# Optimization experiments

Hardware: AMD Instinct MI355X
Metric: run time of the kernel (lower is better)

Reference implementation:

```python
import jax, jax.numpy as jnp
import numpy as np

N, E, D, H = 100000, 600000, 128, 512  # nodes, edges, latent_dim, 4*latent_dim


def setup_inputs() -> dict:
    key = jax.random.key(0)
    ks = jax.random.split(key, 9)
    s = 0.05
    return {
        "z": jax.random.normal(ks[0], (N, D), dtype=jnp.float32),
        "edge_index": jax.random.randint(ks[1], (2, E), 0, N, dtype=jnp.int64),
        "Wg": jax.random.normal(ks[2], (D, D), dtype=jnp.float32) * s,
        "Ws": jax.random.normal(ks[3], (D, D), dtype=jnp.float32) * s,
        "bg": jnp.zeros((D,), dtype=jnp.float32),
        "W1": jax.random.normal(ks[4], (D, H), dtype=jnp.float32) * s,
        "b1": jnp.zeros((H,), dtype=jnp.float32),
        "W2": jax.random.normal(ks[5], (H, H), dtype=jnp.float32) * s,
        "b2": jnp.zeros((H,), dtype=jnp.float32),
        "W3": jax.random.normal(ks[6], (H, D), dtype=jnp.float32) * s,
        "b3": jnp.zeros((D,), dtype=jnp.float32),
    }


def reference(z, edge_index, Wg, Ws, bg, W1, b1, W2, b2, W3, b3):
    src, dst = edge_index[0], edge_index[1]
    n = z.shape[0]
    # GNN: gather neighbor features along edges, mean-aggregate at dst
    msgs = z[src]                                   # (E, D) gather
    agg = jax.ops.segment_sum(msgs, dst, num_segments=n)  # (N, D) scatter-add
    deg = jax.ops.segment_sum(jnp.ones((src.shape[0],), z.dtype), dst, num_segments=n)
    agg = agg / jnp.maximum(deg, 1.0)[:, None]      # mean aggregation
    h = jax.nn.relu(agg @ Wg + z @ Ws + bg)          # (N, D) graph conv output
    # MLP: Linear -> Tanh -> Linear -> Tanh -> Linear
    h = jnp.tanh(h @ W1 + b1)
    h = jnp.tanh(h @ W2 + b2)
    return h @ W3 + b3                               # dz/dt: (N, D)
```

## Files before the change

### kernel.cpp

```cpp
#include <hip/hip_runtime.h>
#include <hip/hip_fp16.h>


typedef _Float16 f16;
typedef __attribute__((ext_vector_type(4))) _Float16 f16x4;
typedef __attribute__((ext_vector_type(8))) _Float16 f16x8;
typedef __attribute__((ext_vector_type(4))) float f32x4;

__device__ __forceinline__ void async_load16(const void* g, void* lds) {
  __builtin_amdgcn_global_load_lds(
      (const __attribute__((address_space(1))) void*)g,
      (__attribute__((address_space(3))) void*)lds, 16, 0, 0);
}

__device__ __forceinline__ float fast_tanh(float x) {
  float a = fabsf(x);
  float e = __expf(-2.0f * a);
  float r = (1.0f - e) * __builtin_amdgcn_rcpf(1.0f + e);
  return copysignf(r, x);
}

__global__ __launch_bounds__(256) void zero_kernel(int* __restrict__ p, int n) {
  int i = blockIdx.x * 256 + threadIdx.x;
  int stride = gridDim.x * 256;
  for (; i < n; i += stride) p[i] = 0;
}

__global__ __launch_bounds__(256) void scan_partial(const int* __restrict__ degi,
                                                    int* __restrict__ bsum, int N) {
  __shared__ int lds[256];
  int b = blockIdx.x, t = threadIdx.x;
  int s = 0;
#pragma unroll
  for (int j = 0; j < 4; ++j) {
    int idx = b * 1024 + t * 4 + j;
    if (idx < N) s += degi[idx];
  }
  lds[t] = s;
  __syncthreads();
  for (int off = 128; off > 0; off >>= 1) {
    if (t < off) lds[t] += lds[t + off];
    __syncthreads();
  }
  if (t == 0) bsum[b] = lds[0];
}

__global__ void scan_bsums(const int* __restrict__ bsum, int* __restrict__ boff,
                           int* __restrict__ row_start, int nb, int N) {
  if (threadIdx.x == 0 && blockIdx.x == 0) {
    int acc = 0;
    for (int i = 0; i < nb; ++i) { boff[i] = acc; acc += bsum[i]; }
    row_start[N] = acc;
  }
}

__global__ __launch_bounds__(256) void scan_final(
    const int* __restrict__ degi, const int* __restrict__ boff,
    int* __restrict__ row_start, int* __restrict__ cursor, int N) {
  __shared__ int lds[256];
  int b = blockIdx.x, t = threadIdx.x;
  int base = b * 1024;
  int v[4];
  int s = 0;
#pragma unroll
  for (int j = 0; j < 4; ++j) {
    int idx = base + t * 4 + j;
    v[j] = (idx < N) ? degi[idx] : 0;
    s += v[j];
  }
  lds[t] = s;
  __syncthreads();
  for (int off = 1; off < 256; off <<= 1) {
    int x = lds[t];
    int y = (t >= off) ? lds[t - off] : 0;
    __syncthreads();
    lds[t] = x + y;
    __syncthreads();
  }
  int pre = boff[b] + lds[t] - s;
#pragma unroll
  for (int j = 0; j < 4; ++j) {
    int idx = base + t * 4 + j;
    if (idx < N) { row_start[idx] = pre; cursor[idx] = pre; pre += v[j]; }
  }
}

__global__ __launch_bounds__(256) void fill_adj(const int* __restrict__ src,
                                                const int* __restrict__ dst,
                                                int* __restrict__ cursor,
                                                int* __restrict__ adj, int E) {
  int e = blockIdx.x * 256 + threadIdx.x;
  if (e >= E) return;
  int p = atomicAdd(&cursor[dst[e]], 1);
  adj[p] = src[e];
}

__global__ __launch_bounds__(256) void fused_prep(
    const int* __restrict__ dst, int* __restrict__ degi, int E,
    const float* __restrict__ Wg, const float* __restrict__ Ws,
    const float* __restrict__ W1, const float* __restrict__ W2,
    const float* __restrict__ W3, f16* __restrict__ wgs, f16* __restrict__ wt1,
    f16* __restrict__ wt2, f16* __restrict__ wt3,
    const float* __restrict__ z, f16* __restrict__ z16, f16* __restrict__ Xc,
    int n4) {
  int i0 = blockIdx.x * 256 + threadIdx.x;
  int stride = gridDim.x * 256;
  for (int i = i0; i < n4; i += stride) {
    float4 v = *(const float4*)(z + 4 * (long long)i);
    f16x4 c;
    c[0] = (f16)v.x; c[1] = (f16)v.y; c[2] = (f16)v.z; c[3] = (f16)v.w;
    *(f16x4*)(z16 + 4 * (long long)i) = c;
    int node = i >> 5, sl = i & 31;
    *(f16x4*)(Xc + (long long)node * 256 + 128 + 4 * sl) = c;
  }
  for (int i = i0; i < E; i += stride) atomicAdd(&degi[dst[i]], 1);
  for (int i = i0; i < 425984; i += stride) {
    if (i < 32768) {
      int n = i >> 8, k = i & 255;
      wgs[i] = (f16)((k < 128) ? Wg[k * 128 + n] : Ws[(k - 128) * 128 + n]);
    } else if (i < 98304) {
      int j = i - 32768, c = j >> 7, k = j & 127;
      wt1[j] = (f16)W1[k * 512 + c];
    } else if (i < 360448) {
      int j = i - 98304, c = j >> 9, k = j & 511;
      wt2[j] = (f16)W2[k * 512 + c];
    } else {
      int j = i - 360448, c = j >> 9, k = j & 511;
      wt3[j] = (f16)W3[k * 128 + c];
    }
  }
}

__global__ __launch_bounds__(256) void gather_xcat(
    const f16* __restrict__ z16, const int* __restrict__ row_start,
    const int* __restrict__ adj, f16* __restrict__ Xc, int N) {
  int node = (blockIdx.x * 256 + threadIdx.x) >> 5;
  if (node >= N) return;
  int lane = threadIdx.x & 31;
  int beg = row_start[node], end = row_start[node + 1];
  float a0 = 0, a1 = 0, a2 = 0, a3 = 0;
#pragma unroll
  for (int j = 0; j < 8; ++j) {
    int idx = beg + j;
    bool vld = idx < end;
    int nb = vld ? adj[idx] : node;
    f16x4 x = *(const f16x4*)(z16 + (long long)nb * 128 + 4 * lane);
    float w = vld ? 1.0f : 0.0f;
    a0 += w * (float)x[0]; a1 += w * (float)x[1];
    a2 += w * (float)x[2]; a3 += w * (float)x[3];
  }
  int i = beg + 8;
  if (i < end) {
    float b0 = 0, b1 = 0, b2 = 0, b3 = 0;
    float c0 = 0, c1 = 0, c2 = 0, c3 = 0;
    float d0 = 0, d1 = 0, d2 = 0, d3 = 0;
    for (; i + 4 <= end; i += 4) {
      int n0 = adj[i], n1 = adj[i + 1], n2 = adj[i + 2], n3 = adj[i + 3];
      f16x4 v0 = *(const f16x4*)(z16 + (long long)n0 * 128 + 4 * lane);
      f16x4 v1 = *(const f16x4*)(z16 + (long long)n1 * 128 + 4 * lane);
      f16x4 v2 = *(const f16x4*)(z16 + (long long)n2 * 128 + 4 * lane);
      f16x4 v3 = *(const f16x4*)(z16 + (long long)n3 * 128 + 4 * lane);
      a0 += (float)v0[0]; a1 += (float)v0[1]; a2 += (float)v0[2]; a3 += (float)v0[3];
      b0 += (float)v1[0]; b1 += (float)v1[1]; b2 += (float)v1[2]; b3 += (float)v1[3];
      c0 += (float)v2[0]; c1 += (float)v2[1]; c2 += (float)v2[2]; c3 += (float)v2[3];
      d0 += (float)v3[0]; d1 += (float)v3[1]; d2 += (float)v3[2]; d3 += (float)v3[3];
    }
    for (; i < end; ++i) {
      f16x4 v = *(const f16x4*)(z16 + (long long)adj[i] * 128 + 4 * lane);
      a0 += (float)v[0]; a1 += (float)v[1]; a2 += (float)v[2]; a3 += (float)v[3];
    }
    a0 += b0 + c0 + d0; a1 += b1 + c1 + d1;
    a2 += b2 + c2 + d2; a3 += b3 + c3 + d3;
  }
  int dg = end - beg;
  float inv = 1.0f / (float)(dg > 1 ? dg : 1);
  long long o = (long long)node * 256;
  f16x4 m;
  m[0] = (f16)(a0 * inv); m[1] = (f16)(a1 * inv);
  m[2] = (f16)(a2 * inv); m[3] = (f16)(a3 * inv);
  *(f16x4*)(Xc + o + 4 * lane) = m;
}

__global__ __launch_bounds__(256) void fused12(
    const f16* __restrict__ Xc, const f16* __restrict__ wgs,
    const f16* __restrict__ wt1, const float* __restrict__ bg,
    const float* __restrict__ b1, f16* __restrict__ h2) {
  __shared__ __align__(16) char L[49152];
  const int tid = threadIdx.x;
  const int wid = tid >> 6, lane = tid & 63;
  const int wm = wid & 1, wn = wid >> 1;
  const int lr = lane & 15, lq = lane >> 4;
  const int key = lr & 7;
  const long long m0 = (long long)blockIdx.x * 128;
  const f16* Ag = Xc + m0 * 256;

  f32x4 acc[4][4];
#pragma unroll
  for (int i = 0; i < 4; ++i)
#pragma unroll
    for (int j = 0; j < 4; ++j)
#pragma unroll
      for (int r = 0; r < 4; ++r) acc[i][j][r] = 0.0f;

#pragma unroll 1
  for (int k0 = 0; k0 < 256; k0 += 64) {
#pragma unroll
    for (int c = 0; c < 4; ++c) {
      int f = c * 256 + tid;
      int row = f >> 3, ss = (f & 7) ^ (row & 7);
      async_load16(Ag + (long long)row * 256 + k0 + ss * 8, L + f * 16);
    }
#pragma unroll
    for (int c = 0; c < 4; ++c) {
      int f = c * 256 + tid;
      int row = f >> 3, ss = (f & 7) ^ (row & 7);
      async_load16(wgs + row * 256 + k0 + ss * 8, L + 16384 + f * 16);
    }
    __syncthreads();
#pragma unroll
    for (int kk = 0; kk < 64; kk += 32) {
      const int co = (((kk >> 3) + lq) ^ key) * 16;
      f16x8 a[4], b[4];
#pragma unroll
      for (int i = 0; i < 4; ++i)
        a[i] = *reinterpret_cast<const f16x8*>(L + (wm * 64 + i * 16 + lr) * 128 + co);
#pragma unroll
      for (int j = 0; j < 4; ++j)
        b[j] = *reinterpret_cast<const f16x8*>(L + 16384 + (wn * 64 + j * 16 + lr) * 128 + co);
#pragma unroll
      for (int i = 0; i < 4; ++i)
#pragma unroll
        for (int j = 0; j < 4; ++j)
          acc[i][j] = __builtin_amdgcn_mfma_f32_16x16x32_f16(a[i], b[j], acc[i][j], 0, 0, 0);
    }
    __syncthreads();
  }

#pragma unroll
  for (int i = 0; i < 4; ++i)
#pragma unroll
    for (int j = 0; j < 4; ++j) {
      int col = wn * 64 + j * 16 + lr;
      float bv = bg[col];
#pragma unroll
      for (int r = 0; r < 4; ++r) {
        int row = wm * 64 + i * 16 + lq * 4 + r;
        float v = fmaxf(acc[i][j][r] + bv, 0.0f);
        *reinterpret_cast<f16*>(L + row * 256 + (((col >> 3) ^ (row & 7)) * 16) +
                                (col & 7) * 2) = (f16)v;
      }
    }
  __syncthreads();

#pragma unroll 1
  for (int cb = 0; cb < 4; ++cb) {
#pragma unroll
    for (int i = 0; i < 4; ++i)
#pragma unroll
      for (int j = 0; j < 4; ++j)
#pragma unroll
        for (int r = 0; r < 4; ++r) acc[i][j][r] = 0.0f;

#pragma unroll 1
    for (int kc = 0; kc < 2; ++kc) {
#pragma unroll
      for (int c = 0; c < 4; ++c) {
        int f = c * 256 + tid;
        int row = f >> 3, ss = (f & 7) ^ (row & 7);
        async_load16(wt1 + (long long)(cb * 128 + row) * 128 + kc * 64 + ss * 8,
                     L + 32768 + f * 16);
      }
      __syncthreads();
#pragma unroll
      for (int kk = 0; kk < 64; kk += 32) {
        const int aslot = kc * 8 + (kk >> 3) + lq;
        const int bco = (((kk >> 3) + lq) ^ key) * 16;
        f16x8 a[4], b[4];
#pragma unroll
        for (int i = 0; i < 4; ++i)
          a[i] = *reinterpret_cast<const f16x8*>(
              L + (wm * 64 + i * 16 + lr) * 256 + (aslot ^ key) * 16);
#pragma unroll
        for (int j = 0; j < 4; ++j)
          b[j] = *reinterpret_cast<const f16x8*>(
              L + 32768 + (wn * 64 + j * 16 + lr) * 128 + bco);
#pragma unroll
        for (int i = 0; i < 4; ++i)
#pragma unroll
          for (int j = 0; j < 4; ++j)
            acc[i][j] = __builtin_amdgcn_mfma_f32_16x16x32_f16(a[i], b[j], acc[i][j], 0, 0, 0);
      }
      __syncthreads();
    }
#pragma unroll
    for (int i = 0; i < 4; ++i)
#pragma unroll
      for (int j = 0; j < 4; ++j) {
        int colg = cb * 128 + wn * 64 + j * 16 + lr;
        float bv = b1[colg];
#pragma unroll
        for (int r = 0; r < 4; ++r) {
          long long row = m0 + wm * 64 + i * 16 + lq * 4 + r;
          h2[row * 512 + colg] = (f16)fast_tanh(acc[i][j][r] + bv);
        }
      }
  }
}

template <int K, int NOUT, int WM, int WN, int MI, int ACT, bool OUTF32>
__global__ __launch_bounds__(WM * WN * 64) void gemm_r(
    const f16* __restrict__ X, const f16* __restrict__ Wt,
    const float* __restrict__ bias, void* __restrict__ OutV, int M) {
  constexpr int NJ = 4;
  constexpr int BM = WM * MI * 16;
  constexpr int BN = WN * NJ * 16;
  constexpr int NTHR = WM * WN * 64;
  constexpr int CA = (BM * 128) / (NTHR * 16);
  constexpr int CB = (BN * 128) / (NTHR * 16);
  __shared__ __align__(16) f16 As[BM * 64];
  __shared__ __align__(16) f16 Bs[BN * 64];

  const int tid = threadIdx.x;
  const int wid = tid >> 6, lane = tid & 63;
  const int wm = wid / WN, wn = wid % WN;
  const int lr = lane & 15, lq = lane >> 4;
  const int rxor = lr & 7;
  const long long m0 = (long long)blockIdx.x * BM;
  const int n0 = blockIdx.y * BN;

  const f16* Ag = X + m0 * K;
  const f16* Bg = Wt + (long long)n0 * K;

  long long aOff[CA], bOff[CB];
#pragma unroll
  for (int c = 0; c < CA; ++c) {
    int f = c * NTHR + tid;
    int row = f >> 3, ss = (f & 7) ^ (row & 7);
    aOff[c] = (long long)row * K + ss * 8;
  }
#pragma unroll
  for (int c = 0; c < CB; ++c) {
    int f = c * NTHR + tid;
    int row = f >> 3, ss = (f & 7) ^ (row & 7);
    bOff[c] = (long long)row * K + ss * 8;
  }

  f32x4 acc[MI][NJ];
#pragma unroll
  for (int i = 0; i < MI; ++i)
#pragma unroll
    for (int j = 0; j < NJ; ++j)
#pragma unroll
      for (int r = 0; r < 4; ++r) acc[i][j][r] = 0.0f;

#pragma unroll 1
  for (int k0 = 0; k0 < K; k0 += 64) {
#pragma unroll
    for (int c = 0; c < CA; ++c)
      async_load16(Ag + aOff[c] + k0, (char*)As + c * NTHR * 16 + wid * 1024);
#pragma unroll
    for (int c = 0; c < CB; ++c)
      async_load16(Bg + bOff[c] + k0, (char*)Bs + c * NTHR * 16 + wid * 1024);
    __syncthreads();
#pragma unroll
    for (int kk = 0; kk < 64; kk += 32) {
      const int co = (((kk >> 3) + lq) ^ rxor) * 16;
      f16x8 a[MI], b[NJ];
#pragma unroll
      for (int i = 0; i < MI; ++i)
        a[i] = *reinterpret_cast<const f16x8*>(
            (const char*)As + (wm * MI * 16 + i * 16 + lr) * 128 + co);
#pragma unroll
      for (int j = 0; j < NJ; ++j)
        b[j] = *reinterpret_cast<const f16x8*>(
            (const char*)Bs + (wn * NJ * 16 + j * 16 + lr) * 128 + co);
#pragma unroll
      for (int i = 0; i < MI; ++i)
#pragma unroll
        for (int j = 0; j < NJ; ++j)
          acc[i][j] = __builtin_amdgcn_mfma_f32_16x16x32_f16(a[i], b[j], acc[i][j], 0, 0, 0);
    }
    __syncthreads();
  }

#pragma unroll
  for (int i = 0; i < MI; ++i) {
#pragma unroll
    for (int j = 0; j < NJ; ++j) {
      int col = n0 + wn * NJ * 16 + j * 16 + lr;
      float bv = bias[col];
#pragma unroll
      for (int r = 0; r < 4; ++r) {
        long long row = m0 + wm * MI * 16 + i * 16 + lq * 4 + r;
        if (row < M) {
          float v = acc[i][j][r] + bv;
          if (ACT == 1) v = fmaxf(v, 0.0f);
          else if (ACT == 2) v = fast_tanh(v);
          if constexpr (OUTF32)
            ((float*)OutV)[row * NOUT + col] = v;
          else
            ((f16*)OutV)[row * NOUT + col] = (f16)v;
        }
      }
    }
  }
}

extern "C" void kernel_launch(void* const* d_in, const int* in_sizes, int n_in,
                              void* d_out, int out_size, void* d_ws, size_t ws_size,
                              hipStream_t stream) {
  const float* z  = (const float*)d_in[0];
  const int*   ei = (const int*)d_in[1];
  const float* Wg = (const float*)d_in[2];
  const float* Ws = (const float*)d_in[3];
  const float* bg = (const float*)d_in[4];
  const float* W1 = (const float*)d_in[5];
  const float* b1 = (const float*)d_in[6];
  const float* W2 = (const float*)d_in[7];
  const float* b2 = (const float*)d_in[8];
  const float* W3 = (const float*)d_in[9];
  const float* b3 = (const float*)d_in[10];

  const int Nn = in_sizes[0] / 128;
  const int E  = in_sizes[1] / 2;
  const int* src = ei;
  const int* dst = ei + E;
  const int nb = (Nn + 1023) / 1024;
  const int gm128 = (Nn + 127) / 128;
  const long long Mpad = (long long)gm128 * 128;

  char* base = (char*)d_ws;
  const size_t XCB = (size_t)Mpad * 256 * 2;
  const size_t H3B = (size_t)Mpad * 512 * 2;
  f16* Xc = (f16*)(base);
  f16* h3 = (f16*)(base);
  size_t off = XCB;
  auto alloc = [&](size_t b) -> void* {
    void* p = base + off;
    off += (b + 255) & ~(size_t)255;
    return p;
  };
  int* degi      = (int*)alloc((size_t)Nn * 4);
  int* row_start = (int*)alloc((size_t)(Nn + 1) * 4);
  int* cursor    = (int*)alloc((size_t)Nn * 4);
  int* adj       = (int*)alloc((size_t)(E + 8) * 4);
  int* bsum      = (int*)alloc((size_t)nb * 4);
  int* boff      = (int*)alloc((size_t)nb * 4);
  f16* z16       = (f16*)alloc((size_t)Nn * 128 * 2);
  off = H3B;
  f16* h2  = (f16*)alloc((size_t)Mpad * 512 * 2);
  f16* wgs = (f16*)alloc((size_t)128 * 256 * 2);
  f16* wt1 = (f16*)alloc((size_t)512 * 128 * 2);
  f16* wt2 = (f16*)alloc((size_t)512 * 512 * 2);
  f16* wt3 = (f16*)alloc((size_t)128 * 512 * 2);

  zero_kernel<<<(Nn + 255) / 256, 256, 0, stream>>>(degi, Nn);
  fused_prep<<<2048, 256, 0, stream>>>(dst, degi, E, Wg, Ws, W1, W2, W3,
                                       wgs, wt1, wt2, wt3, z, z16, Xc, Nn * 32);
  scan_partial<<<nb, 256, 0, stream>>>(degi, bsum, Nn);
  scan_bsums<<<1, 64, 0, stream>>>(bsum, boff, row_start, nb, Nn);
  scan_final<<<nb, 256, 0, stream>>>(degi, boff, row_start, cursor, Nn);
  fill_adj<<<(E + 255) / 256, 256, 0, stream>>>(src, dst, cursor, adj, E);

  {
    long long tot = (long long)Nn * 32;
    gather_xcat<<<(int)((tot + 255) / 256), 256, 0, stream>>>(z16, row_start, adj, Xc, Nn);
  }

  fused12<<<gm128, 256, 0, stream>>>(Xc, wgs, wt1, bg, b1, h2);
  gemm_r<512, 512, 2, 4, 4, 2, false><<<dim3(gm128, 2), 512, 0, stream>>>(h2, wt2, b2, (void*)h3, Nn);
  gemm_r<512, 128, 2, 2, 4, 0, true><<<dim3(gm128, 1), 256, 0, stream>>>(h3, wt3, b3, d_out, Nn);
}
```

Baseline: 323.0 us.

## Fold block-offset scan into scan_final, memset degrees, enlarge GEMM row tiles

Removes the single-thread scan_bsums kernel: each scan_final block now reduces the preceding block sums itself in LDS, and row_start[N] is set directly to E. The zero kernel becomes hipMemsetAsync. The two later GEMMs switch to 256-row tiles with doubled thread counts (1024 and 512), with Mpad padded to 256. The aims are fewer launches, no serial scan, and more reuse of each weight tile, at the cost of fewer blocks and heavier per-block register and LDS use.

```diff
diff --git a/kernel.cpp b/kernel.cpp
--- a/kernel.cpp
+++ b/kernel.cpp
@@ -20,12 +20,6 @@
   return copysignf(r, x);
 }
 
-__global__ __launch_bounds__(256) void zero_kernel(int* __restrict__ p, int n) {
-  int i = blockIdx.x * 256 + threadIdx.x;
-  int stride = gridDim.x * 256;
-  for (; i < n; i += stride) p[i] = 0;
-}
-
 __global__ __launch_bounds__(256) void scan_partial(const int* __restrict__ degi,
                                                     int* __restrict__ bsum, int N) {
   __shared__ int lds[256];
@@ -45,20 +39,24 @@
   if (t == 0) bsum[b] = lds[0];
 }
 
-__global__ void scan_bsums(const int* __restrict__ bsum, int* __restrict__ boff,
-                           int* __restrict__ row_start, int nb, int N) {
-  if (threadIdx.x == 0 && blockIdx.x == 0) {
-    int acc = 0;
-    for (int i = 0; i < nb; ++i) { boff[i] = acc; acc += bsum[i]; }
-    row_start[N] = acc;
-  }
-}
-
 __global__ __launch_bounds__(256) void scan_final(
-    const int* __restrict__ degi, const int* __restrict__ boff,
-    int* __restrict__ row_start, int* __restrict__ cursor, int N) {
+    const int* __restrict__ degi, const int* __restrict__ bsum,
+    int* __restrict__ row_start, int* __restrict__ cursor, int nb, int N, int E) {
   __shared__ int lds[256];
+  __shared__ int sboff;
   int b = blockIdx.x, t = threadIdx.x;
+  lds[t] = (t < b && t < nb) ? bsum[t] : 0;
+  __syncthreads();
+  for (int off = 128; off > 0; off >>= 1) {
+    if (t < off) lds[t] += lds[t + off];
+    __syncthreads();
+  }
+  if (t == 0) {
+    sboff = lds[0];
+    if (b == 0) row_start[N] = E;
+  }
+  __syncthreads();
+
   int base = b * 1024;
   int v[4];
   int s = 0;
@@ -77,7 +75,7 @@
     lds[t] = x + y;
     __syncthreads();
   }
-  int pre = boff[b] + lds[t] - s;
+  int pre = sboff + lds[t] - s;
 #pragma unroll
   for (int j = 0; j < 4; ++j) {
     int idx = base + t * 4 + j;
@@ -426,8 +424,9 @@
   const int* src = ei;
   const int* dst = ei + E;
   const int nb = (Nn + 1023) / 1024;
-  const int gm128 = (Nn + 127) / 128;
-  const long long Mpad = (long long)gm128 * 128;
+  const int gm256 = (Nn + 255) / 256;
+  const long long Mpad = (long long)gm256 * 256;
+  const int gm128 = gm256 * 2;
 
   char* base = (char*)d_ws;
   const size_t XCB = (size_t)Mpad * 256 * 2;
@@ -445,7 +444,6 @@
   int* cursor    = (int*)alloc((size_t)Nn * 4);
   int* adj       = (int*)alloc((size_t)(E + 8) * 4);
   int* bsum      = (int*)alloc((size_t)nb * 4);
-  int* boff      = (int*)alloc((size_t)nb * 4);
   f16* z16       = (f16*)alloc((size_t)Nn * 128 * 2);
   off = H3B;
   f16* h2  = (f16*)alloc((size_t)Mpad * 512 * 2);
@@ -454,12 +452,11 @@
   f16* wt2 = (f16*)alloc((size_t)512 * 512 * 2);
   f16* wt3 = (f16*)alloc((size_t)128 * 512 * 2);
 
-  zero_kernel<<<(Nn + 255) / 256, 256, 0, stream>>>(degi, Nn);
+  hipMemsetAsync(degi, 0, (size_t)Nn * 4, stream);
   fused_prep<<<2048, 256, 0, stream>>>(dst, degi, E, Wg, Ws, W1, W2, W3,
                                        wgs, wt1, wt2, wt3, z, z16, Xc, Nn * 32);
   scan_partial<<<nb, 256, 0, stream>>>(degi, bsum, Nn);
-  scan_bsums<<<1, 64, 0, stream>>>(bsum, boff, row_start, nb, Nn);
-  scan_final<<<nb, 256, 0, stream>>>(degi, boff, row_start, cursor, Nn);
+  scan_final<<<nb, 256, 0, stream>>>(degi, bsum, row_start, cursor, nb, Nn, E);
   fill_adj<<<(E + 255) / 256, 256, 0, stream>>>(src, dst, cursor, adj, E);
 
   {
@@ -468,6 +465,6 @@
   }
 
   fused12<<<gm128, 256, 0, stream>>>(Xc, wgs, wt1, bg, b1, h2);
-  gemm_r<512, 512, 2, 4, 4, 2, false><<<dim3(gm128, 2), 512, 0, stream>>>(h2, wt2, b2, (void*)h3, Nn);
-  gemm_r<512, 128, 2, 2, 4, 0, true><<<dim3(gm128, 1), 256, 0, stream>>>(h3, wt3, b3, d_out, Nn);
-}
+  gemm_r<512, 512, 4, 4, 4, 2, false><<<dim3(gm256, 2), 1024, 0, stream>>>(h2, wt2, b2, (void*)h3, Nn);
+  gemm_r<512, 128, 4, 2, 4, 0, true><<<dim3(gm256, 1), 512, 0, stream>>>(h3, wt3, b3, d_out, Nn);
+}
```

New measurement: 318.1 us. No clear change (-1.5%).
